# Kernel optimization log

Measured on AMD Instinct MI355X. Metric: run time of the kernel, lower is better.

The kernel has to match this reference:

```python
import jax, jax.numpy as jnp
import numpy as np

B, K, D = 8192, 50, 64
NU, NV = 100000, 100000


def setup_inputs() -> dict:
    key = jax.random.key(0)
    ks = jax.random.split(key, 9)
    nodes = jax.random.randint(ks[0], (B,), 0, NU)
    history = jax.random.randint(ks[1], (B, K), 0, NV)
    degrees = jax.random.randint(ks[2], (B,), 1, K + 1)  # 1..K actual neighbors per node
    u_to_e = jax.random.normal(ks[3], (NU, D), dtype=jnp.float32)
    v_to_e = jax.random.normal(ks[4], (NV, D), dtype=jnp.float32)
    s1 = 1.0 / np.sqrt(2 * D)
    s2 = 1.0 / np.sqrt(D)
    att1_w = jax.random.normal(ks[5], (D, 2 * D), dtype=jnp.float32) * s1
    att2_w = jax.random.normal(ks[6], (D, D), dtype=jnp.float32) * s2
    att3_w = jax.random.normal(ks[7], (1, D), dtype=jnp.float32) * s2
    return {
        "nodes": nodes, "history": history, "degrees": degrees,
        "u_to_e": u_to_e, "v_to_e": v_to_e,
        "att1_w": att1_w, "att1_b": jnp.zeros((D,), jnp.float32),
        "att2_w": att2_w, "att2_b": jnp.zeros((D,), jnp.float32),
        "att3_w": att3_w, "att3_b": jnp.zeros((1,), jnp.float32),
    }


def reference(nodes, history, degrees, u_to_e, v_to_e,
              att1_w, att1_b, att2_w, att2_b, att3_w, att3_b):
    # uv=True: neighbors are items (v_to_e), self representation from u_to_e.
    neigh = v_to_e[history]                      # [B, K, D] gathered neighbor embeddings
    self_e = u_to_e[nodes]                       # [B, D]
    self_rep = jnp.broadcast_to(self_e[:, None, :], neigh.shape)
    x = jnp.concatenate([neigh, self_rep], axis=-1)        # [B, K, 2D]
    h = jax.nn.relu(jnp.einsum('bkf,df->bkd', x, att1_w) + att1_b)
    h = jax.nn.relu(jnp.einsum('bkd,ed->bke', h, att2_w) + att2_b)
    logits = (jnp.einsum('bkd,od->bko', h, att3_w) + att3_b)[..., 0]  # [B, K]
    # Softmax over the true (ragged) neighbor set only.
    mask = jnp.arange(K)[None, :] < degrees[:, None]       # [B, K] bool
    logits = jnp.where(mask, logits, -1e9)
    att = jax.nn.softmax(logits, axis=1) * mask            # [B, K]
    return jnp.einsum('bkd,bk->bd', neigh, att)            # [B, D]
```

## Files before the change

### kernel.cpp

```cpp
#include <hip/hip_runtime.h>
#include <cstdint>
#include <cstddef>

constexpr int D = 64;
constexpr int TWO_D = 128;

typedef __attribute__((ext_vector_type(8))) short bf16x8;
typedef __attribute__((ext_vector_type(4))) float f32x4;
typedef __attribute__((ext_vector_type(4))) unsigned short u16x4;

static __device__ __forceinline__ short f2bf(float x) {
    unsigned u = __builtin_bit_cast(unsigned, x);
    u += 0x7fffu + ((u >> 16) & 1u);
    return (short)(u >> 16);
}
static __device__ __forceinline__ float bf2f(short h) {
    return __builtin_bit_cast(float, ((unsigned)(unsigned short)h) << 16);
}

__global__ __launch_bounds__(256) void proj_gemm(
    const float* __restrict__ v_to_e, const float* __restrict__ u_to_e,
    const int* __restrict__ nodes,
    const float* __restrict__ att1_w, const float* __restrict__ att1_b,
    const float* __restrict__ att2_w,
    unsigned short* __restrict__ P16, float* __restrict__ S,
    unsigned short* __restrict__ W2F,
    int NV, int Bn, int nPB)
{
    const int tid = threadIdx.x;

    if ((int)blockIdx.x == nPB + (Bn + 63) / 64) {
        if (tid < 64) {
            const int plg = tid >> 4, plc = tid & 15;
#pragma unroll
            for (int tc = 0; tc < 4; ++tc)
#pragma unroll
                for (int ks = 0; ks < 2; ++ks) {
                    const float* src =
                        att2_w + (tc * 16 + plc) * D + ks * 32 + plg * 8;
                    const float4 a = *(const float4*)src;
                    const float4 c = *(const float4*)(src + 4);
                    bf16x8 f;
                    f[0] = f2bf(a.x); f[1] = f2bf(a.y);
                    f[2] = f2bf(a.z); f[3] = f2bf(a.w);
                    f[4] = f2bf(c.x); f[5] = f2bf(c.y);
                    f[6] = f2bf(c.z); f[7] = f2bf(c.w);
                    *(bf16x8*)(W2F + ((size_t)(tc * 2 + ks) * 64 + tid) * 8) = f;
                }
        }
        return;
    }

    constexpr int ST = 68;
    __shared__ float xs[64 * ST];
    __shared__ float ws[64 * ST];

    const bool isS = ((int)blockIdx.x >= nPB);
    const int base = (isS ? ((int)blockIdx.x - nPB) : (int)blockIdx.x) * 64;
    const int nRows = isS ? Bn : NV;
    const int woff  = isS ? D : 0;
    const float* X  = isS ? u_to_e : v_to_e;

#pragma unroll
    for (int it = 0; it < 4; ++it) {
        const int flat = it * 256 + tid;
        const int dd = flat >> 4, f4 = flat & 15;
        const float4 w = *(const float4*)(att1_w + dd * TWO_D + woff + f4 * 4);
        ws[(f4 * 4 + 0) * ST + dd] = w.x;
        ws[(f4 * 4 + 1) * ST + dd] = w.y;
        ws[(f4 * 4 + 2) * ST + dd] = w.z;
        ws[(f4 * 4 + 3) * ST + dd] = w.w;
    }
#pragma unroll
    for (int it = 0; it < 4; ++it) {
        const int flat = it * 256 + tid;
        const int r = flat >> 4, f4 = flat & 15;
        int gr = base + r;
        if (gr >= nRows) gr = nRows - 1;
        const int row = isS ? nodes[gr] : gr;
        const float4 x = *(const float4*)(X + (size_t)row * D + f4 * 4);
        xs[(f4 * 4 + 0) * ST + r] = x.x;
        xs[(f4 * 4 + 1) * ST + r] = x.y;
        xs[(f4 * 4 + 2) * ST + r] = x.z;
        xs[(f4 * 4 + 3) * ST + r] = x.w;
    }
    __syncthreads();

    const int d0 = (tid & 15) * 4;
    const int r0 = (tid >> 4) * 4;
    float acc[4][4];
#pragma unroll
    for (int i = 0; i < 4; ++i)
#pragma unroll
        for (int j = 0; j < 4; ++j) acc[i][j] = 0.f;

#pragma unroll 8
    for (int f = 0; f < D; ++f) {
        const float4 w = *(const float4*)&ws[f * ST + d0];
        const float4 x = *(const float4*)&xs[f * ST + r0];
        const float wv[4] = {w.x, w.y, w.z, w.w};
        const float xv[4] = {x.x, x.y, x.z, x.w};
#pragma unroll
        for (int ri = 0; ri < 4; ++ri)
#pragma unroll
            for (int di = 0; di < 4; ++di)
                acc[ri][di] += xv[ri] * wv[di];
    }

    if (isS) {
        float bv[4];
#pragma unroll
        for (int di = 0; di < 4; ++di) bv[di] = att1_b[d0 + di];
#pragma unroll
        for (int ri = 0; ri < 4; ++ri) {
            const int gr = base + r0 + ri;
            if (gr < nRows) {
                float4 o = {acc[ri][0] + bv[0], acc[ri][1] + bv[1],
                            acc[ri][2] + bv[2], acc[ri][3] + bv[3]};
                *(float4*)(S + (size_t)gr * D + d0) = o;
            }
        }
    } else {
#pragma unroll
        for (int ri = 0; ri < 4; ++ri) {
            const int gr = base + r0 + ri;
            if (gr < nRows) {
                u16x4 o;
                o[0] = (unsigned short)f2bf(acc[ri][0]);
                o[1] = (unsigned short)f2bf(acc[ri][1]);
                o[2] = (unsigned short)f2bf(acc[ri][2]);
                o[3] = (unsigned short)f2bf(acc[ri][3]);
                *(u16x4*)(P16 + (size_t)gr * D + d0) = o;
            }
        }
    }
}

__global__ __launch_bounds__(256) void agg_mfma(
    const int* __restrict__ history, const int* __restrict__ degrees,
    const float* __restrict__ v_to_e,
    const float* __restrict__ att2_b, const float* __restrict__ att3_w,
    const unsigned short* __restrict__ P16, const float* __restrict__ S,
    const unsigned short* __restrict__ W2F,
    float* __restrict__ out, int Bn, int K)
{
    __shared__ float red[4][64];
    __shared__ float mxs[4];
    __shared__ float sms[4];

    const int b     = (int)blockIdx.x;
    const int wslot = threadIdx.x >> 6;
    const int l     = threadIdx.x & 63;
    const int lg    = l >> 4;
    const int lc    = l & 15;
    const int deg   = degrees[b];
    const bool live = (wslot * 16 < deg);
    const bool act  = (wslot * 16 + lc < deg);

    int kk = wslot * 16 + lc;
    if (kk > K - 1) kk = K - 1;
    const int vrow = history[(size_t)b * K + kk];

    float4 vr4[4];
    if (live) {
#pragma unroll
        for (int jj = 0; jj < 4; ++jj) {
            const int row = __shfl(vrow, jj * 4 + lg);
            vr4[jj] = *(const float4*)(v_to_e + (size_t)row * D + lc * 4);
        }
    }

    float m_w = -1e30f, ex = 0.f;
    float4 acc4 = {0.f, 0.f, 0.f, 0.f};
    if (live) {
        const bf16x8 praw0 = *(const bf16x8*)(P16 + (size_t)vrow * D + lg * 8);
        const bf16x8 praw1 = *(const bf16x8*)(P16 + (size_t)vrow * D + 32 + lg * 8);
        const float* sp = S + (size_t)b * D;
        const float4 s00 = *(const float4*)(sp + lg * 8);
        const float4 s01 = *(const float4*)(sp + lg * 8 + 4);
        const float4 s10 = *(const float4*)(sp + 32 + lg * 8);
        const float4 s11 = *(const float4*)(sp + 32 + lg * 8 + 4);

        bf16x8 af0, af1;
        af0[0] = f2bf(fmaxf(bf2f(praw0[0]) + s00.x, 0.f));
        af0[1] = f2bf(fmaxf(bf2f(praw0[1]) + s00.y, 0.f));
        af0[2] = f2bf(fmaxf(bf2f(praw0[2]) + s00.z, 0.f));
        af0[3] = f2bf(fmaxf(bf2f(praw0[3]) + s00.w, 0.f));
        af0[4] = f2bf(fmaxf(bf2f(praw0[4]) + s01.x, 0.f));
        af0[5] = f2bf(fmaxf(bf2f(praw0[5]) + s01.y, 0.f));
        af0[6] = f2bf(fmaxf(bf2f(praw0[6]) + s01.z, 0.f));
        af0[7] = f2bf(fmaxf(bf2f(praw0[7]) + s01.w, 0.f));
        af1[0] = f2bf(fmaxf(bf2f(praw1[0]) + s10.x, 0.f));
        af1[1] = f2bf(fmaxf(bf2f(praw1[1]) + s10.y, 0.f));
        af1[2] = f2bf(fmaxf(bf2f(praw1[2]) + s10.z, 0.f));
        af1[3] = f2bf(fmaxf(bf2f(praw1[3]) + s10.w, 0.f));
        af1[4] = f2bf(fmaxf(bf2f(praw1[4]) + s11.x, 0.f));
        af1[5] = f2bf(fmaxf(bf2f(praw1[5]) + s11.y, 0.f));
        af1[6] = f2bf(fmaxf(bf2f(praw1[6]) + s11.z, 0.f));
        af1[7] = f2bf(fmaxf(bf2f(praw1[7]) + s11.w, 0.f));

        f32x4 acc[4];
#pragma unroll
        for (int tc = 0; tc < 4; ++tc) acc[tc] = (f32x4)0.f;
#pragma unroll
        for (int tc = 0; tc < 4; ++tc) {
            const bf16x8 w0 = *(const bf16x8*)(
                W2F + ((size_t)(tc * 2 + 0) * 64 + l) * 8);
            acc[tc] = __builtin_amdgcn_mfma_f32_16x16x32_bf16(
                w0, af0, acc[tc], 0, 0, 0);
            const bf16x8 w1 = *(const bf16x8*)(
                W2F + ((size_t)(tc * 2 + 1) * 64 + l) * 8);
            acc[tc] = __builtin_amdgcn_mfma_f32_16x16x32_bf16(
                w1, af1, acc[tc], 0, 0, 0);
        }

        float part = 0.f;
#pragma unroll
        for (int tc = 0; tc < 4; ++tc) {
            const float4 b2v = *(const float4*)(att2_b + tc * 16 + lg * 4);
            const float4 w3v = *(const float4*)(att3_w + tc * 16 + lg * 4);
            part += fmaxf(acc[tc][0] + b2v.x, 0.f) * w3v.x;
            part += fmaxf(acc[tc][1] + b2v.y, 0.f) * w3v.y;
            part += fmaxf(acc[tc][2] + b2v.z, 0.f) * w3v.z;
            part += fmaxf(acc[tc][3] + b2v.w, 0.f) * w3v.w;
        }
        part += __shfl_xor(part, 16);
        part += __shfl_xor(part, 32);
        const float logit = act ? part : -1e30f;

        m_w = logit;
#pragma unroll
        for (int off = 1; off < 16; off <<= 1)
            m_w = fmaxf(m_w, __shfl_xor(m_w, off));
        ex = act ? __expf(logit - m_w) : 0.f;
        float s_w = ex;
#pragma unroll
        for (int off = 1; off < 16; off <<= 1)
            s_w += __shfl_xor(s_w, off);
        if (l == 0) { mxs[wslot] = m_w; sms[wslot] = s_w; }

#pragma unroll
        for (int jj = 0; jj < 4; ++jj) {
            const float a = __shfl(ex, jj * 4 + lg);
            acc4.x += a * vr4[jj].x;
            acc4.y += a * vr4[jj].y;
            acc4.z += a * vr4[jj].z;
            acc4.w += a * vr4[jj].w;
        }
        acc4.x += __shfl_xor(acc4.x, 16); acc4.x += __shfl_xor(acc4.x, 32);
        acc4.y += __shfl_xor(acc4.y, 16); acc4.y += __shfl_xor(acc4.y, 32);
        acc4.z += __shfl_xor(acc4.z, 16); acc4.z += __shfl_xor(acc4.z, 32);
        acc4.w += __shfl_xor(acc4.w, 16); acc4.w += __shfl_xor(acc4.w, 32);
    } else {
        if (l == 0) { mxs[wslot] = -1e30f; sms[wslot] = 0.f; }
    }

    __syncthreads();
    const float m = fmaxf(fmaxf(mxs[0], mxs[1]), fmaxf(mxs[2], mxs[3]));
    const float tot = sms[0] * __expf(mxs[0] - m) + sms[1] * __expf(mxs[1] - m)
                    + sms[2] * __expf(mxs[2] - m) + sms[3] * __expf(mxs[3] - m);
    const float scale = live ? __expf(m_w - m) / tot : 0.f;

    const float comp = (lg == 0) ? acc4.x : (lg == 1) ? acc4.y
                     : (lg == 2) ? acc4.z : acc4.w;
    red[wslot][lc * 4 + lg] = comp * scale;
    __syncthreads();
    if (wslot == 0)
        out[(size_t)b * D + l] =
            (red[0][l] + red[1][l]) + (red[2][l] + red[3][l]);
}

__global__ __launch_bounds__(256) void agg_fallback(
    const int* __restrict__ nodes, const int* __restrict__ history,
    const int* __restrict__ degrees,
    const float* __restrict__ u_to_e, const float* __restrict__ v_to_e,
    const float* __restrict__ att1_w, const float* __restrict__ att1_b,
    const float* __restrict__ att2_w, const float* __restrict__ att2_b,
    const float* __restrict__ att3_w, const float* __restrict__ att3_b,
    float* __restrict__ out, int Bn, int K)
{
    const int b    = (int)((blockIdx.x * blockDim.x + threadIdx.x) >> 6);
    const int lane = threadIdx.x & 63;
    if (b >= Bn) return;

    const int  deg    = degrees[b];
    const bool active = (lane < deg);
    const int  v      = history[(size_t)b * K + ((lane < K) ? lane : 0)];

    float h1[D];
    float vr[D];
    const float4* v4 = (const float4*)(v_to_e + (size_t)v * D);
#pragma unroll
    for (int i = 0; i < D / 4; ++i) {
        float4 t = v4[i];
        vr[4 * i + 0] = t.x; vr[4 * i + 1] = t.y;
        vr[4 * i + 2] = t.z; vr[4 * i + 3] = t.w;
    }
    const float* urow = u_to_e + (size_t)nodes[b] * D;
#pragma unroll
    for (int d = 0; d < D; ++d) {
        const float* w1 = att1_w + d * TWO_D;
        float a0 = att1_b[d], a1 = 0.f, a2 = 0.f, a3 = 0.f;
#pragma unroll
        for (int f = 0; f < D; f += 4) {
            a0 += vr[f + 0] * w1[f + 0];
            a1 += vr[f + 1] * w1[f + 1];
            a2 += vr[f + 2] * w1[f + 2];
            a3 += vr[f + 3] * w1[f + 3];
            a0 += urow[f + 0] * w1[D + f + 0];
            a1 += urow[f + 1] * w1[D + f + 1];
            a2 += urow[f + 2] * w1[D + f + 2];
            a3 += urow[f + 3] * w1[D + f + 3];
        }
        h1[d] = fmaxf((a0 + a1) + (a2 + a3), 0.f);
    }

    float logit = att3_b[0];
#pragma unroll 4
    for (int e = 0; e < D; ++e) {
        const float* w2r = att2_w + e * D;
        float a0 = 0.f, a1 = 0.f, a2 = 0.f, a3 = 0.f;
#pragma unroll
        for (int dd = 0; dd < D; dd += 4) {
            a0 += h1[dd + 0] * w2r[dd + 0];
            a1 += h1[dd + 1] * w2r[dd + 1];
            a2 += h1[dd + 2] * w2r[dd + 2];
            a3 += h1[dd + 3] * w2r[dd + 3];
        }
        float h2 = (a0 + a1) + (a2 + a3) + att2_b[e];
        logit += fmaxf(h2, 0.f) * att3_w[e];
    }

    float ml = active ? logit : -1e30f;
#pragma unroll
    for (int off = 32; off > 0; off >>= 1) ml = fmaxf(ml, __shfl_xor(ml, off));
    const float ex = active ? __expf(logit - ml) : 0.f;
    float smv = ex;
#pragma unroll
    for (int off = 32; off > 0; off >>= 1) smv += __shfl_xor(smv, off);
    const float att = ex / smv;

    float acc = 0.f;
    for (int kk = 0; kk < deg; ++kk) {
        const float a  = __shfl(att, kk);
        const int   vk = __shfl(v, kk);
        acc += a * v_to_e[(size_t)vk * D + lane];
    }
    out[(size_t)b * D + lane] = acc;
}

extern "C" void kernel_launch(void* const* d_in, const int* in_sizes, int n_in,
                              void* d_out, int out_size, void* d_ws, size_t ws_size,
                              hipStream_t stream)
{
    const int*   nodes   = (const int*)d_in[0];
    const int*   history = (const int*)d_in[1];
    const int*   degrees = (const int*)d_in[2];
    const float* u_to_e  = (const float*)d_in[3];
    const float* v_to_e  = (const float*)d_in[4];
    const float* att1_w  = (const float*)d_in[5];
    const float* att1_b  = (const float*)d_in[6];
    const float* att2_w  = (const float*)d_in[7];
    const float* att2_b  = (const float*)d_in[8];
    const float* att3_w  = (const float*)d_in[9];
    const float* att3_b  = (const float*)d_in[10];
    float*       out     = (float*)d_out;

    const int Bn = in_sizes[0];
    const int K  = in_sizes[1] / Bn;
    const int NV = in_sizes[4] / D;

    const size_t p16_bytes = (size_t)NV * D * sizeof(unsigned short);
    const size_t s_bytes   = (size_t)Bn * D * sizeof(float);
    const size_t w2f_bytes = (size_t)8 * 64 * 8 * sizeof(unsigned short);
    const size_t need = p16_bytes + s_bytes + w2f_bytes;

    if (ws_size >= need) {
        unsigned short* P16 = (unsigned short*)d_ws;
        float* S = (float*)((char*)d_ws + p16_bytes);
        unsigned short* W2F = (unsigned short*)((char*)d_ws + p16_bytes + s_bytes);
        const int nPB = (NV + 63) / 64;
        const int nSB = (Bn + 63) / 64;
        proj_gemm<<<nPB + nSB + 1, 256, 0, stream>>>(
            v_to_e, u_to_e, nodes, att1_w, att1_b, att2_w,
            P16, S, W2F, NV, Bn, nPB);
        agg_mfma<<<Bn, 256, 0, stream>>>(
            history, degrees, v_to_e, att2_b, att3_w,
            P16, S, W2F, out, Bn, K);
    } else {
        const int agg_blocks = (Bn * 64 + 255) / 256;
        agg_fallback<<<agg_blocks, 256, 0, stream>>>(
            nodes, history, degrees, u_to_e, v_to_e,
            att1_w, att1_b, att2_w, att2_b, att3_w, att3_b,
            out, Bn, K);
    }
}
```

Baseline: 50.35 us.

## Split fused attention aggregation into separate score and value kernels

```diff
diff --git a/kernel.cpp b/kernel.cpp
--- a/kernel.cpp
+++ b/kernel.cpp
@@ -136,15 +136,13 @@
     }
 }
 
-__global__ __launch_bounds__(256) void agg_mfma(
+__global__ __launch_bounds__(256, 8) void score_mfma(
     const int* __restrict__ history, const int* __restrict__ degrees,
-    const float* __restrict__ v_to_e,
     const float* __restrict__ att2_b, const float* __restrict__ att3_w,
     const unsigned short* __restrict__ P16, const float* __restrict__ S,
     const unsigned short* __restrict__ W2F,
-    float* __restrict__ out, int Bn, int K)
+    float* __restrict__ ATT, int Bn, int K)
 {
-    __shared__ float red[4][64];
     __shared__ float mxs[4];
     __shared__ float sms[4];
 
@@ -157,22 +155,12 @@
     const bool live = (wslot * 16 < deg);
     const bool act  = (wslot * 16 + lc < deg);
 
-    int kk = wslot * 16 + lc;
-    if (kk > K - 1) kk = K - 1;
-    const int vrow = history[(size_t)b * K + kk];
-
-    float4 vr4[4];
+    float m_w = -1e30f, ex = 0.f;
     if (live) {
-#pragma unroll
-        for (int jj = 0; jj < 4; ++jj) {
-            const int row = __shfl(vrow, jj * 4 + lg);
-            vr4[jj] = *(const float4*)(v_to_e + (size_t)row * D + lc * 4);
-        }
-    }
-
-    float m_w = -1e30f, ex = 0.f;
-    float4 acc4 = {0.f, 0.f, 0.f, 0.f};
-    if (live) {
+        int kk = wslot * 16 + lc;
+        if (kk > K - 1) kk = K - 1;
+        const int vrow = history[(size_t)b * K + kk];
+
         const bf16x8 praw0 = *(const bf16x8*)(P16 + (size_t)vrow * D + lg * 8);
         const bf16x8 praw1 = *(const bf16x8*)(P16 + (size_t)vrow * D + 32 + lg * 8);
         const float* sp = S + (size_t)b * D;
@@ -199,30 +187,22 @@
         af1[6] = f2bf(fmaxf(bf2f(praw1[6]) + s11.z, 0.f));
         af1[7] = f2bf(fmaxf(bf2f(praw1[7]) + s11.w, 0.f));
 
-        f32x4 acc[4];
-#pragma unroll
-        for (int tc = 0; tc < 4; ++tc) acc[tc] = (f32x4)0.f;
+        float part = 0.f;
 #pragma unroll
         for (int tc = 0; tc < 4; ++tc) {
+            f32x4 acc = (f32x4)0.f;
             const bf16x8 w0 = *(const bf16x8*)(
                 W2F + ((size_t)(tc * 2 + 0) * 64 + l) * 8);
-            acc[tc] = __builtin_amdgcn_mfma_f32_16x16x32_bf16(
-                w0, af0, acc[tc], 0, 0, 0);
+            acc = __builtin_amdgcn_mfma_f32_16x16x32_bf16(w0, af0, acc, 0, 0, 0);
             const bf16x8 w1 = *(const bf16x8*)(
                 W2F + ((size_t)(tc * 2 + 1) * 64 + l) * 8);
-            acc[tc] = __builtin_amdgcn_mfma_f32_16x16x32_bf16(
-                w1, af1, acc[tc], 0, 0, 0);
-        }
-
-        float part = 0.f;
-#pragma unroll
-        for (int tc = 0; tc < 4; ++tc) {
+            acc = __builtin_amdgcn_mfma_f32_16x16x32_bf16(w1, af1, acc, 0, 0, 0);
             const float4 b2v = *(const float4*)(att2_b + tc * 16 + lg * 4);
             const float4 w3v = *(const float4*)(att3_w + tc * 16 + lg * 4);
-            part += fmaxf(acc[tc][0] + b2v.x, 0.f) * w3v.x;
-            part += fmaxf(acc[tc][1] + b2v.y, 0.f) * w3v.y;
-            part += fmaxf(acc[tc][2] + b2v.z, 0.f) * w3v.z;
-            part += fmaxf(acc[tc][3] + b2v.w, 0.f) * w3v.w;
+            part += fmaxf(acc[0] + b2v.x, 0.f) * w3v.x;
+            part += fmaxf(acc[1] + b2v.y, 0.f) * w3v.y;
+            part += fmaxf(acc[2] + b2v.z, 0.f) * w3v.z;
+            part += fmaxf(acc[3] + b2v.w, 0.f) * w3v.w;
         }
         part += __shfl_xor(part, 16);
         part += __shfl_xor(part, 32);
@@ -238,19 +218,6 @@
         for (int off = 1; off < 16; off <<= 1)
             s_w += __shfl_xor(s_w, off);
         if (l == 0) { mxs[wslot] = m_w; sms[wslot] = s_w; }
-
-#pragma unroll
-        for (int jj = 0; jj < 4; ++jj) {
-            const float a = __shfl(ex, jj * 4 + lg);
-            acc4.x += a * vr4[jj].x;
-            acc4.y += a * vr4[jj].y;
-            acc4.z += a * vr4[jj].z;
-            acc4.w += a * vr4[jj].w;
-        }
-        acc4.x += __shfl_xor(acc4.x, 16); acc4.x += __shfl_xor(acc4.x, 32);
-        acc4.y += __shfl_xor(acc4.y, 16); acc4.y += __shfl_xor(acc4.y, 32);
-        acc4.z += __shfl_xor(acc4.z, 16); acc4.z += __shfl_xor(acc4.z, 32);
-        acc4.w += __shfl_xor(acc4.w, 16); acc4.w += __shfl_xor(acc4.w, 32);
     } else {
         if (l == 0) { mxs[wslot] = -1e30f; sms[wslot] = 0.f; }
     }
@@ -260,10 +227,50 @@
     const float tot = sms[0] * __expf(mxs[0] - m) + sms[1] * __expf(mxs[1] - m)
                     + sms[2] * __expf(mxs[2] - m) + sms[3] * __expf(mxs[3] - m);
     const float scale = live ? __expf(m_w - m) / tot : 0.f;
+    if (lg == 0)
+        ATT[(size_t)b * 64 + wslot * 16 + lc] = ex * scale;
+}
+
+__global__ __launch_bounds__(256, 8) void value_kernel(
+    const int* __restrict__ history, const int* __restrict__ degrees,
+    const float* __restrict__ v_to_e, const float* __restrict__ ATT,
+    float* __restrict__ out, int Bn, int K)
+{
+    __shared__ float red[4][64];
+
+    const int b     = (int)blockIdx.x;
+    const int wslot = threadIdx.x >> 6;
+    const int l     = threadIdx.x & 63;
+    const int lg    = l >> 4;
+    const int lc    = l & 15;
+    const int deg   = degrees[b];
+
+    int kk = wslot * 16 + lc;
+    if (kk > K - 1) kk = K - 1;
+    const int vrow = history[(size_t)b * K + kk];
+    const float att = ATT[(size_t)b * 64 + wslot * 16 + lc];
+
+    float4 acc4 = {0.f, 0.f, 0.f, 0.f};
+#pragma unroll
+    for (int jj = 0; jj < 4; ++jj) {
+        if (wslot * 16 + jj * 4 < deg) {
+            const int   row = __shfl(vrow, jj * 4 + lg);
+            const float a   = __shfl(att,  jj * 4 + lg);
+            const float4 v = *(const float4*)(v_to_e + (size_t)row * D + lc * 4);
+            acc4.x += a * v.x;
+            acc4.y += a * v.y;
+            acc4.z += a * v.z;
+            acc4.w += a * v.w;
+        }
+    }
+    acc4.x += __shfl_xor(acc4.x, 16); acc4.x += __shfl_xor(acc4.x, 32);
+    acc4.y += __shfl_xor(acc4.y, 16); acc4.y += __shfl_xor(acc4.y, 32);
+    acc4.z += __shfl_xor(acc4.z, 16); acc4.z += __shfl_xor(acc4.z, 32);
+    acc4.w += __shfl_xor(acc4.w, 16); acc4.w += __shfl_xor(acc4.w, 32);
 
     const float comp = (lg == 0) ? acc4.x : (lg == 1) ? acc4.y
                      : (lg == 2) ? acc4.z : acc4.w;
-    red[wslot][lc * 4 + lg] = comp * scale;
+    red[wslot][lc * 4 + lg] = comp;
     __syncthreads();
     if (wslot == 0)
         out[(size_t)b * D + l] =
@@ -373,20 +380,25 @@
     const size_t p16_bytes = (size_t)NV * D * sizeof(unsigned short);
     const size_t s_bytes   = (size_t)Bn * D * sizeof(float);
     const size_t w2f_bytes = (size_t)8 * 64 * 8 * sizeof(unsigned short);
-    const size_t need = p16_bytes + s_bytes + w2f_bytes;
+    const size_t att_bytes = (size_t)Bn * 64 * sizeof(float);
+    const size_t need = p16_bytes + s_bytes + w2f_bytes + att_bytes;
 
     if (ws_size >= need) {
-        unsigned short* P16 = (unsigned short*)d_ws;
-        float* S = (float*)((char*)d_ws + p16_bytes);
-        unsigned short* W2F = (unsigned short*)((char*)d_ws + p16_bytes + s_bytes);
+        char* p = (char*)d_ws;
+        unsigned short* P16 = (unsigned short*)p;            p += p16_bytes;
+        float*          S   = (float*)p;                     p += s_bytes;
+        unsigned short* W2F = (unsigned short*)p;            p += w2f_bytes;
+        float*          ATT = (float*)p;
         const int nPB = (NV + 63) / 64;
         const int nSB = (Bn + 63) / 64;
         proj_gemm<<<nPB + nSB + 1, 256, 0, stream>>>(
             v_to_e, u_to_e, nodes, att1_w, att1_b, att2_w,
             P16, S, W2F, NV, Bn, nPB);
-        agg_mfma<<<Bn, 256, 0, stream>>>(
-            history, degrees, v_to_e, att2_b, att3_w,
-            P16, S, W2F, out, Bn, K);
+        score_mfma<<<Bn, 256, 0, stream>>>(
+            history, degrees, att2_b, att3_w,
+            P16, S, W2F, ATT, Bn, K);
+        value_kernel<<<Bn, 256, 0, stream>>>(
+            history, degrees, v_to_e, ATT, out, Bn, K);
     } else {
         const int agg_blocks = (Bn * 64 + 255) / 256;
         agg_fallback<<<agg_blocks, 256, 0, stream>>>(
```

Measured after the change: 57.72 us. 14.6% more time.

## Compute first-layer projection with bf16 MFMA instead of FP32 LDS GEMM

Applied to the files above, without the earlier changes.

```diff
diff --git a/kernel.cpp b/kernel.cpp
--- a/kernel.cpp
+++ b/kernel.cpp
@@ -17,8 +17,16 @@
 static __device__ __forceinline__ float bf2f(short h) {
     return __builtin_bit_cast(float, ((unsigned)(unsigned short)h) << 16);
 }
-
-__global__ __launch_bounds__(256) void proj_gemm(
+static __device__ __forceinline__ bf16x8 cvt8(const float* p) {
+    const float4 a = *(const float4*)p;
+    const float4 c = *(const float4*)(p + 4);
+    bf16x8 f;
+    f[0] = f2bf(a.x); f[1] = f2bf(a.y); f[2] = f2bf(a.z); f[3] = f2bf(a.w);
+    f[4] = f2bf(c.x); f[5] = f2bf(c.y); f[6] = f2bf(c.z); f[7] = f2bf(c.w);
+    return f;
+}
+
+__global__ __launch_bounds__(256) void proj_mfma(
     const float* __restrict__ v_to_e, const float* __restrict__ u_to_e,
     const int* __restrict__ nodes,
     const float* __restrict__ att1_w, const float* __restrict__ att1_b,
@@ -36,24 +44,13 @@
             for (int tc = 0; tc < 4; ++tc)
 #pragma unroll
                 for (int ks = 0; ks < 2; ++ks) {
-                    const float* src =
-                        att2_w + (tc * 16 + plc) * D + ks * 32 + plg * 8;
-                    const float4 a = *(const float4*)src;
-                    const float4 c = *(const float4*)(src + 4);
-                    bf16x8 f;
-                    f[0] = f2bf(a.x); f[1] = f2bf(a.y);
-                    f[2] = f2bf(a.z); f[3] = f2bf(a.w);
-                    f[4] = f2bf(c.x); f[5] = f2bf(c.y);
-                    f[6] = f2bf(c.z); f[7] = f2bf(c.w);
+                    const bf16x8 f =
+                        cvt8(att2_w + (tc * 16 + plc) * D + ks * 32 + plg * 8);
                     *(bf16x8*)(W2F + ((size_t)(tc * 2 + ks) * 64 + tid) * 8) = f;
                 }
         }
         return;
     }
-
-    constexpr int ST = 68;
-    __shared__ float xs[64 * ST];
-    __shared__ float ws[64 * ST];
 
     const bool isS = ((int)blockIdx.x >= nPB);
     const int base = (isS ? ((int)blockIdx.x - nPB) : (int)blockIdx.x) * 64;
@@ -61,76 +58,55 @@
     const int woff  = isS ? D : 0;
     const float* X  = isS ? u_to_e : v_to_e;
 
-#pragma unroll
-    for (int it = 0; it < 4; ++it) {
-        const int flat = it * 256 + tid;
-        const int dd = flat >> 4, f4 = flat & 15;
-        const float4 w = *(const float4*)(att1_w + dd * TWO_D + woff + f4 * 4);
-        ws[(f4 * 4 + 0) * ST + dd] = w.x;
-        ws[(f4 * 4 + 1) * ST + dd] = w.y;
-        ws[(f4 * 4 + 2) * ST + dd] = w.z;
-        ws[(f4 * 4 + 3) * ST + dd] = w.w;
-    }
-#pragma unroll
-    for (int it = 0; it < 4; ++it) {
-        const int flat = it * 256 + tid;
-        const int r = flat >> 4, f4 = flat & 15;
-        int gr = base + r;
-        if (gr >= nRows) gr = nRows - 1;
-        const int row = isS ? nodes[gr] : gr;
-        const float4 x = *(const float4*)(X + (size_t)row * D + f4 * 4);
-        xs[(f4 * 4 + 0) * ST + r] = x.x;
-        xs[(f4 * 4 + 1) * ST + r] = x.y;
-        xs[(f4 * 4 + 2) * ST + r] = x.z;
-        xs[(f4 * 4 + 3) * ST + r] = x.w;
-    }
-    __syncthreads();
-
-    const int d0 = (tid & 15) * 4;
-    const int r0 = (tid >> 4) * 4;
-    float acc[4][4];
-#pragma unroll
-    for (int i = 0; i < 4; ++i)
-#pragma unroll
-        for (int j = 0; j < 4; ++j) acc[i][j] = 0.f;
-
-#pragma unroll 8
-    for (int f = 0; f < D; ++f) {
-        const float4 w = *(const float4*)&ws[f * ST + d0];
-        const float4 x = *(const float4*)&xs[f * ST + r0];
-        const float wv[4] = {w.x, w.y, w.z, w.w};
-        const float xv[4] = {x.x, x.y, x.z, x.w};
-#pragma unroll
-        for (int ri = 0; ri < 4; ++ri)
-#pragma unroll
-            for (int di = 0; di < 4; ++di)
-                acc[ri][di] += xv[ri] * wv[di];
+    const int w  = tid >> 6;
+    const int l  = tid & 63;
+    const int lg = l >> 4;
+    const int lc = l & 15;
+
+    bf16x8 w1f[4][2];
+#pragma unroll
+    for (int tc = 0; tc < 4; ++tc)
+#pragma unroll
+        for (int ks = 0; ks < 2; ++ks)
+            w1f[tc][ks] = cvt8(
+                att1_w + (tc * 16 + lc) * TWO_D + woff + ks * 32 + lg * 8);
+
+    int grow = base + w * 16 + lc;
+    if (grow >= nRows) grow = nRows - 1;
+    const int xrow = isS ? nodes[grow] : grow;
+    const float* xp = X + (size_t)xrow * D;
+    bf16x8 a0 = cvt8(xp + lg * 8);
+    bf16x8 a1 = cvt8(xp + 32 + lg * 8);
+
+    f32x4 acc[4];
+#pragma unroll
+    for (int tc = 0; tc < 4; ++tc) acc[tc] = (f32x4)0.f;
+#pragma unroll
+    for (int tc = 0; tc < 4; ++tc) {
+        acc[tc] = __builtin_amdgcn_mfma_f32_16x16x32_bf16(a0, w1f[tc][0], acc[tc], 0, 0, 0);
+        acc[tc] = __builtin_amdgcn_mfma_f32_16x16x32_bf16(a1, w1f[tc][1], acc[tc], 0, 0, 0);
     }
 
     if (isS) {
-        float bv[4];
-#pragma unroll
-        for (int di = 0; di < 4; ++di) bv[di] = att1_b[d0 + di];
-#pragma unroll
-        for (int ri = 0; ri < 4; ++ri) {
-            const int gr = base + r0 + ri;
+#pragma unroll
+        for (int r = 0; r < 4; ++r) {
+            const int gr = base + w * 16 + lg * 4 + r;
             if (gr < nRows) {
-                float4 o = {acc[ri][0] + bv[0], acc[ri][1] + bv[1],
-                            acc[ri][2] + bv[2], acc[ri][3] + bv[3]};
-                *(float4*)(S + (size_t)gr * D + d0) = o;
+#pragma unroll
+                for (int tc = 0; tc < 4; ++tc)
+                    S[(size_t)gr * D + tc * 16 + lc] =
+                        acc[tc][r] + att1_b[tc * 16 + lc];
             }
         }
     } else {
 #pragma unroll
-        for (int ri = 0; ri < 4; ++ri) {
-            const int gr = base + r0 + ri;
+        for (int r = 0; r < 4; ++r) {
+            const int gr = base + w * 16 + lg * 4 + r;
             if (gr < nRows) {
-                u16x4 o;
-                o[0] = (unsigned short)f2bf(acc[ri][0]);
-                o[1] = (unsigned short)f2bf(acc[ri][1]);
-                o[2] = (unsigned short)f2bf(acc[ri][2]);
-                o[3] = (unsigned short)f2bf(acc[ri][3]);
-                *(u16x4*)(P16 + (size_t)gr * D + d0) = o;
+#pragma unroll
+                for (int tc = 0; tc < 4; ++tc)
+                    P16[(size_t)gr * D + tc * 16 + lc] =
+                        (unsigned short)f2bf(acc[tc][r]);
             }
         }
     }
@@ -381,7 +357,7 @@
         unsigned short* W2F = (unsigned short*)((char*)d_ws + p16_bytes + s_bytes);
         const int nPB = (NV + 63) / 64;
         const int nSB = (Bn + 63) / 64;
-        proj_gemm<<<nPB + nSB + 1, 256, 0, stream>>>(
+        proj_mfma<<<nPB + nSB + 1, 256, 0, stream>>>(
             v_to_e, u_to_e, nodes, att1_w, att1_b, att2_w,
             P16, S, W2F, NV, Bn, nPB);
         agg_mfma<<<Bn, 256, 0, stream>>>(
```

Result: slower. 52.28 us (+3.8%).

## Compute neighbor projection on the fly with MFMA instead of precomputing all items

Applied to the files above, without the earlier changes.

```diff
diff --git a/kernel.cpp b/kernel.cpp
--- a/kernel.cpp
+++ b/kernel.cpp
@@ -14,38 +14,41 @@
     u += 0x7fffu + ((u >> 16) & 1u);
     return (short)(u >> 16);
 }
-static __device__ __forceinline__ float bf2f(short h) {
-    return __builtin_bit_cast(float, ((unsigned)(unsigned short)h) << 16);
-}
-
-__global__ __launch_bounds__(256) void proj_gemm(
-    const float* __restrict__ v_to_e, const float* __restrict__ u_to_e,
-    const int* __restrict__ nodes,
+static __device__ __forceinline__ float bf2f(unsigned short h) {
+    return __builtin_bit_cast(float, ((unsigned)h) << 16);
+}
+static __device__ __forceinline__ bf16x8 cvt8(const float* p) {
+    const float4 a = *(const float4*)p;
+    const float4 c = *(const float4*)(p + 4);
+    bf16x8 f;
+    f[0] = f2bf(a.x); f[1] = f2bf(a.y); f[2] = f2bf(a.z); f[3] = f2bf(a.w);
+    f[4] = f2bf(c.x); f[5] = f2bf(c.y); f[6] = f2bf(c.z); f[7] = f2bf(c.w);
+    return f;
+}
+
+__global__ __launch_bounds__(256) void proj_s(
+    const float* __restrict__ u_to_e, const int* __restrict__ nodes,
     const float* __restrict__ att1_w, const float* __restrict__ att1_b,
     const float* __restrict__ att2_w,
-    unsigned short* __restrict__ P16, float* __restrict__ S,
+    float* __restrict__ S, unsigned short* __restrict__ W1F,
     unsigned short* __restrict__ W2F,
-    int NV, int Bn, int nPB)
+    int Bn, int nSB)
 {
     const int tid = threadIdx.x;
 
-    if ((int)blockIdx.x == nPB + (Bn + 63) / 64) {
+    if ((int)blockIdx.x == nSB) {
         if (tid < 64) {
             const int plg = tid >> 4, plc = tid & 15;
 #pragma unroll
             for (int tc = 0; tc < 4; ++tc)
 #pragma unroll
                 for (int ks = 0; ks < 2; ++ks) {
-                    const float* src =
-                        att2_w + (tc * 16 + plc) * D + ks * 32 + plg * 8;
-                    const float4 a = *(const float4*)src;
-                    const float4 c = *(const float4*)(src + 4);
-                    bf16x8 f;
-                    f[0] = f2bf(a.x); f[1] = f2bf(a.y);
-                    f[2] = f2bf(a.z); f[3] = f2bf(a.w);
-                    f[4] = f2bf(c.x); f[5] = f2bf(c.y);
-                    f[6] = f2bf(c.z); f[7] = f2bf(c.w);
-                    *(bf16x8*)(W2F + ((size_t)(tc * 2 + ks) * 64 + tid) * 8) = f;
+                    const bf16x8 f1 = cvt8(
+                        att1_w + (tc * 16 + plc) * TWO_D + ks * 32 + plg * 8);
+                    *(bf16x8*)(W1F + ((size_t)(tc * 2 + ks) * 64 + tid) * 8) = f1;
+                    const bf16x8 f2 = cvt8(
+                        att2_w + (tc * 16 + plc) * D + ks * 32 + plg * 8);
+                    *(bf16x8*)(W2F + ((size_t)(tc * 2 + ks) * 64 + tid) * 8) = f2;
                 }
         }
         return;
@@ -55,17 +58,13 @@
     __shared__ float xs[64 * ST];
     __shared__ float ws[64 * ST];
 
-    const bool isS = ((int)blockIdx.x >= nPB);
-    const int base = (isS ? ((int)blockIdx.x - nPB) : (int)blockIdx.x) * 64;
-    const int nRows = isS ? Bn : NV;
-    const int woff  = isS ? D : 0;
-    const float* X  = isS ? u_to_e : v_to_e;
+    const int base = (int)blockIdx.x * 64;
 
 #pragma unroll
     for (int it = 0; it < 4; ++it) {
         const int flat = it * 256 + tid;
         const int dd = flat >> 4, f4 = flat & 15;
-        const float4 w = *(const float4*)(att1_w + dd * TWO_D + woff + f4 * 4);
+        const float4 w = *(const float4*)(att1_w + dd * TWO_D + D + f4 * 4);
         ws[(f4 * 4 + 0) * ST + dd] = w.x;
         ws[(f4 * 4 + 1) * ST + dd] = w.y;
         ws[(f4 * 4 + 2) * ST + dd] = w.z;
@@ -76,9 +75,9 @@
         const int flat = it * 256 + tid;
         const int r = flat >> 4, f4 = flat & 15;
         int gr = base + r;
-        if (gr >= nRows) gr = nRows - 1;
-        const int row = isS ? nodes[gr] : gr;
-        const float4 x = *(const float4*)(X + (size_t)row * D + f4 * 4);
+        if (gr >= Bn) gr = Bn - 1;
+        const int row = nodes[gr];
+        const float4 x = *(const float4*)(u_to_e + (size_t)row * D + f4 * 4);
         xs[(f4 * 4 + 0) * ST + r] = x.x;
         xs[(f4 * 4 + 1) * ST + r] = x.y;
         xs[(f4 * 4 + 2) * ST + r] = x.z;
@@ -107,43 +106,30 @@
                 acc[ri][di] += xv[ri] * wv[di];
     }
 
-    if (isS) {
-        float bv[4];
-#pragma unroll
-        for (int di = 0; di < 4; ++di) bv[di] = att1_b[d0 + di];
-#pragma unroll
-        for (int ri = 0; ri < 4; ++ri) {
-            const int gr = base + r0 + ri;
-            if (gr < nRows) {
-                float4 o = {acc[ri][0] + bv[0], acc[ri][1] + bv[1],
-                            acc[ri][2] + bv[2], acc[ri][3] + bv[3]};
-                *(float4*)(S + (size_t)gr * D + d0) = o;
-            }
-        }
-    } else {
-#pragma unroll
-        for (int ri = 0; ri < 4; ++ri) {
-            const int gr = base + r0 + ri;
-            if (gr < nRows) {
-                u16x4 o;
-                o[0] = (unsigned short)f2bf(acc[ri][0]);
-                o[1] = (unsigned short)f2bf(acc[ri][1]);
-                o[2] = (unsigned short)f2bf(acc[ri][2]);
-                o[3] = (unsigned short)f2bf(acc[ri][3]);
-                *(u16x4*)(P16 + (size_t)gr * D + d0) = o;
-            }
-        }
-    }
-}
-
-__global__ __launch_bounds__(256) void agg_mfma(
+    float bv[4];
+#pragma unroll
+    for (int di = 0; di < 4; ++di) bv[di] = att1_b[d0 + di];
+#pragma unroll
+    for (int ri = 0; ri < 4; ++ri) {
+        const int gr = base + r0 + ri;
+        if (gr < Bn) {
+            float4 o = {acc[ri][0] + bv[0], acc[ri][1] + bv[1],
+                        acc[ri][2] + bv[2], acc[ri][3] + bv[3]};
+            *(float4*)(S + (size_t)gr * D + d0) = o;
+        }
+    }
+}
+
+__global__ __launch_bounds__(256) void agg_fused(
     const int* __restrict__ history, const int* __restrict__ degrees,
     const float* __restrict__ v_to_e,
     const float* __restrict__ att2_b, const float* __restrict__ att3_w,
-    const unsigned short* __restrict__ P16, const float* __restrict__ S,
+    const float* __restrict__ S,
+    const unsigned short* __restrict__ W1F,
     const unsigned short* __restrict__ W2F,
     float* __restrict__ out, int Bn, int K)
 {
+    __shared__ unsigned short hldsb[4][16 * 72];
     __shared__ float red[4][64];
     __shared__ float mxs[4];
     __shared__ float sms[4];
@@ -173,56 +159,48 @@
     float m_w = -1e30f, ex = 0.f;
     float4 acc4 = {0.f, 0.f, 0.f, 0.f};
     if (live) {
-        const bf16x8 praw0 = *(const bf16x8*)(P16 + (size_t)vrow * D + lg * 8);
-        const bf16x8 praw1 = *(const bf16x8*)(P16 + (size_t)vrow * D + 32 + lg * 8);
-        const float* sp = S + (size_t)b * D;
-        const float4 s00 = *(const float4*)(sp + lg * 8);
-        const float4 s01 = *(const float4*)(sp + lg * 8 + 4);
-        const float4 s10 = *(const float4*)(sp + 32 + lg * 8);
-        const float4 s11 = *(const float4*)(sp + 32 + lg * 8 + 4);
-
-        bf16x8 af0, af1;
-        af0[0] = f2bf(fmaxf(bf2f(praw0[0]) + s00.x, 0.f));
-        af0[1] = f2bf(fmaxf(bf2f(praw0[1]) + s00.y, 0.f));
-        af0[2] = f2bf(fmaxf(bf2f(praw0[2]) + s00.z, 0.f));
-        af0[3] = f2bf(fmaxf(bf2f(praw0[3]) + s00.w, 0.f));
-        af0[4] = f2bf(fmaxf(bf2f(praw0[4]) + s01.x, 0.f));
-        af0[5] = f2bf(fmaxf(bf2f(praw0[5]) + s01.y, 0.f));
-        af0[6] = f2bf(fmaxf(bf2f(praw0[6]) + s01.z, 0.f));
-        af0[7] = f2bf(fmaxf(bf2f(praw0[7]) + s01.w, 0.f));
-        af1[0] = f2bf(fmaxf(bf2f(praw1[0]) + s10.x, 0.f));
-        af1[1] = f2bf(fmaxf(bf2f(praw1[1]) + s10.y, 0.f));
-        af1[2] = f2bf(fmaxf(bf2f(praw1[2]) + s10.z, 0.f));
-        af1[3] = f2bf(fmaxf(bf2f(praw1[3]) + s10.w, 0.f));
-        af1[4] = f2bf(fmaxf(bf2f(praw1[4]) + s11.x, 0.f));
-        af1[5] = f2bf(fmaxf(bf2f(praw1[5]) + s11.y, 0.f));
-        af1[6] = f2bf(fmaxf(bf2f(praw1[6]) + s11.z, 0.f));
-        af1[7] = f2bf(fmaxf(bf2f(praw1[7]) + s11.w, 0.f));
-
-        f32x4 acc[4];
-#pragma unroll
-        for (int tc = 0; tc < 4; ++tc) acc[tc] = (f32x4)0.f;
+        const float* vp = v_to_e + (size_t)vrow * D;
+        const bf16x8 bv0 = cvt8(vp + lg * 8);
+        const bf16x8 bv1 = cvt8(vp + 32 + lg * 8);
+
+        unsigned short* hrow = &hldsb[wslot][0];
 #pragma unroll
         for (int tc = 0; tc < 4; ++tc) {
+            f32x4 hacc = (f32x4)0.f;
+            const bf16x8 w10 = *(const bf16x8*)(
+                W1F + ((size_t)(tc * 2 + 0) * 64 + l) * 8);
+            hacc = __builtin_amdgcn_mfma_f32_16x16x32_bf16(w10, bv0, hacc, 0, 0, 0);
+            const bf16x8 w11 = *(const bf16x8*)(
+                W1F + ((size_t)(tc * 2 + 1) * 64 + l) * 8);
+            hacc = __builtin_amdgcn_mfma_f32_16x16x32_bf16(w11, bv1, hacc, 0, 0, 0);
+            const float4 sv = *(const float4*)(S + (size_t)b * D + tc * 16 + lg * 4);
+            u16x4 hb;
+            hb[0] = (unsigned short)f2bf(fmaxf(hacc[0] + sv.x, 0.f));
+            hb[1] = (unsigned short)f2bf(fmaxf(hacc[1] + sv.y, 0.f));
+            hb[2] = (unsigned short)f2bf(fmaxf(hacc[2] + sv.z, 0.f));
+            hb[3] = (unsigned short)f2bf(fmaxf(hacc[3] + sv.w, 0.f));
+            *(u16x4*)&hrow[lc * 72 + tc * 16 + lg * 4] = hb;
+        }
+
+        const bf16x8 af0 = *(const bf16x8*)&hrow[lc * 72 + lg * 8];
+        const bf16x8 af1 = *(const bf16x8*)&hrow[lc * 72 + 32 + lg * 8];
+
+        float part = 0.f;
+#pragma unroll
+        for (int tc = 0; tc < 4; ++tc) {
+            f32x4 acc = (f32x4)0.f;
             const bf16x8 w0 = *(const bf16x8*)(
                 W2F + ((size_t)(tc * 2 + 0) * 64 + l) * 8);
-            acc[tc] = __builtin_amdgcn_mfma_f32_16x16x32_bf16(
-                w0, af0, acc[tc], 0, 0, 0);
+            acc = __builtin_amdgcn_mfma_f32_16x16x32_bf16(w0, af0, acc, 0, 0, 0);
             const bf16x8 w1 = *(const bf16x8*)(
                 W2F + ((size_t)(tc * 2 + 1) * 64 + l) * 8);
-            acc[tc] = __builtin_amdgcn_mfma_f32_16x16x32_bf16(
-                w1, af1, acc[tc], 0, 0, 0);
-        }
-
-        float part = 0.f;
-#pragma unroll
-        for (int tc = 0; tc < 4; ++tc) {
+            acc = __builtin_amdgcn_mfma_f32_16x16x32_bf16(w1, af1, acc, 0, 0, 0);
             const float4 b2v = *(const float4*)(att2_b + tc * 16 + lg * 4);
             const float4 w3v = *(const float4*)(att3_w + tc * 16 + lg * 4);
-            part += fmaxf(acc[tc][0] + b2v.x, 0.f) * w3v.x;
-            part += fmaxf(acc[tc][1] + b2v.y, 0.f) * w3v.y;
-            part += fmaxf(acc[tc][2] + b2v.z, 0.f) * w3v.z;
-            part += fmaxf(acc[tc][3] + b2v.w, 0.f) * w3v.w;
+            part += fmaxf(acc[0] + b2v.x, 0.f) * w3v.x;
+            part += fmaxf(acc[1] + b2v.y, 0.f) * w3v.y;
+            part += fmaxf(acc[2] + b2v.z, 0.f) * w3v.z;
+            part += fmaxf(acc[3] + b2v.w, 0.f) * w3v.w;
         }
         part += __shfl_xor(part, 16);
         part += __shfl_xor(part, 32);
@@ -368,25 +346,22 @@
 
     const int Bn = in_sizes[0];
     const int K  = in_sizes[1] / Bn;
-    const int NV = in_sizes[4] / D;
-
-    const size_t p16_bytes = (size_t)NV * D * sizeof(unsigned short);
+
     const size_t s_bytes   = (size_t)Bn * D * sizeof(float);
-    const size_t w2f_bytes = (size_t)8 * 64 * 8 * sizeof(unsigned short);
-    const size_t need = p16_bytes + s_bytes + w2f_bytes;
+    const size_t wf_bytes  = (size_t)8 * 64 * 8 * sizeof(unsigned short);
+    const size_t need = s_bytes + 2 * wf_bytes;
 
     if (ws_size >= need) {
-        unsigned short* P16 = (unsigned short*)d_ws;
-        float* S = (float*)((char*)d_ws + p16_bytes);
-        unsigned short* W2F = (unsigned short*)((char*)d_ws + p16_bytes + s_bytes);
-        const int nPB = (NV + 63) / 64;
+        char* p = (char*)d_ws;
+        float*          S   = (float*)p;            p += s_bytes;
+        unsigned short* W1F = (unsigned short*)p;   p += wf_bytes;
+        unsigned short* W2F = (unsigned short*)p;
         const int nSB = (Bn + 63) / 64;
-        proj_gemm<<<nPB + nSB + 1, 256, 0, stream>>>(
-            v_to_e, u_to_e, nodes, att1_w, att1_b, att2_w,
-            P16, S, W2F, NV, Bn, nPB);
-        agg_mfma<<<Bn, 256, 0, stream>>>(
+        proj_s<<<nSB + 1, 256, 0, stream>>>(
+            u_to_e, nodes, att1_w, att1_b, att2_w, S, W1F, W2F, Bn, nSB);
+        agg_fused<<<Bn, 256, 0, stream>>>(
             history, degrees, v_to_e, att2_b, att3_w,
-            P16, S, W2F, out, Bn, K);
+            S, W1F, W2F, out, Bn, K);
     } else {
         const int agg_blocks = (Bn * 64 + 255) / 256;
         agg_fallback<<<agg_blocks, 256, 0, stream>>>(
```

After: 43.95 us. -12.7%, faster.
